# Kernel optimization log

Hardware: AMD Instinct MI355X
Metric: run time of the kernel (lower is better)

## Reference

```python
import jax, jax.numpy as jnp
import numpy as np

VOCAB, N_CLASS, H, E = 50000, 6, 512, 300
B, S = 256, 512


def setup_inputs() -> dict:
    key = jax.random.key(0)
    ks = jax.random.split(key, 10)
    return {
        "seq": jax.random.randint(ks[0], (B, S), 0, VOCAB),
        "classes": jnp.arange(N_CLASS),
        "embed_W": jax.random.normal(ks[1], (VOCAB, E), jnp.float32) * 0.1,
        "embed_class_W": jax.random.normal(ks[2], (N_CLASS, H), jnp.float32) * 0.1,
        "W_ih": jax.random.normal(ks[3], (3 * H, E), jnp.float32) * 0.05,
        "W_hh": jax.random.normal(ks[4], (3 * H, H), jnp.float32) * 0.05,
        "b_ih": jax.random.normal(ks[5], (3 * H,), jnp.float32) * 0.05,
        "b_hh": jax.random.normal(ks[6], (3 * H,), jnp.float32) * 0.05,
        "attend": jax.random.normal(ks[7], (H, H), jnp.float32) * 0.1,
        "W_cls": jax.random.normal(ks[8], (2, H), jnp.float32) * 0.05,
        "b_cls": jax.random.normal(ks[9], (2,), jnp.float32) * 0.05,
    }


def _gru_scan(xs, W_ih, W_hh, b_ih, b_hh):
    # xs: [S, B, E]; torch GRUCell semantics
    h0 = jnp.zeros((xs.shape[1], W_hh.shape[1]), xs.dtype)

    def step(h, x):
        gi = x @ W_ih.T + b_ih            # [B, 3H]
        gh = h @ W_hh.T + b_hh            # [B, 3H]
        i_r, i_z, i_n = jnp.split(gi, 3, axis=-1)
        h_r, h_z, h_n = jnp.split(gh, 3, axis=-1)
        r = jax.nn.sigmoid(i_r + h_r)
        z = jax.nn.sigmoid(i_z + h_z)
        n = jnp.tanh(i_n + r * h_n)
        h_new = (1.0 - z) * n + z * h
        return h_new, h_new

    _, hs = jax.lax.scan(step, h0, xs)
    return hs  # [S, B, H]


def reference(seq, classes, embed_W, embed_class_W, W_ih, W_hh, b_ih, b_hh,
              attend, W_cls, b_cls):
    pad_mask = (seq > 0).astype(embed_W.dtype)          # [B, S]
    seq_emb = jnp.tanh(embed_W[seq])                    # [B, S, E]
    hs = _gru_scan(seq_emb.transpose(1, 0, 2), W_ih, W_hh, b_ih, b_hh)
    seq_repr = hs.transpose(1, 0, 2)                    # [B, S, H]

    class_emb = embed_class_W[classes]                  # [C, H]
    attn = jnp.tanh(class_emb) @ attend                 # [C, H]
    # scores[c,b,s] = tanh(attn)[c] . seq_repr[b,s], masked
    scores = jnp.einsum('ch,bsh->cbs', jnp.tanh(attn), seq_repr)
    scores = scores * pad_mask[None, :, :]
    ctx = jnp.einsum('cbs,bsh->cbh', jnp.tanh(scores), seq_repr)  # [C, B, H]
    logits = jnp.tanh(ctx) @ W_cls.T + b_cls            # [C, B, 2]
    return jax.nn.log_softmax(logits, axis=-1)
```

## Files before the change

### kernel.cpp

```cpp
#include <hip/hip_runtime.h>
#include <cstdint>
#include <cstddef>

#define NB 256
#define NS 512
#define NE 300
#define NH 512

using f32x4 = __attribute__((ext_vector_type(4))) float;
using s16x8 = __attribute__((ext_vector_type(8))) short;

static __device__ __forceinline__ unsigned short f2bf(float f) {
  unsigned u = __float_as_uint(f);
  u += 0x7FFFu + ((u >> 16) & 1u);
  return (unsigned short)(u >> 16);
}
static __device__ __forceinline__ float bf2f(unsigned short h) {
  return __uint_as_float(((unsigned)h) << 16);
}
static __device__ __forceinline__ float fast_tanh(float x) {
  float xc = fminf(fmaxf(x, -9.f), 9.f);
  float e = __expf(2.f * xc);
  return (e - 1.f) / (e + 1.f);
}
static __device__ __forceinline__ float sigm(float x) {
  return 1.f / (1.f + __expf(-x));
}

__global__ void k_zero(unsigned short* __restrict__ h_ex, unsigned* __restrict__ flags) {
  int i = blockIdx.x * 256 + threadIdx.x;
  f32x4 z = {0.f, 0.f, 0.f, 0.f};
  *(f32x4*)(h_ex + (size_t)i * 16) = z;
  *(f32x4*)(h_ex + (size_t)i * 16 + 8) = z;
  if (i < 512) flags[i] = 0;
}

__global__ __launch_bounds__(256) void k_amat(const int* __restrict__ classes,
                                              const float* __restrict__ ecw,
                                              const float* __restrict__ attend,
                                              unsigned short* __restrict__ a_bf) {
  __shared__ float tc[6][512];
  const int tid = threadIdx.x, j = blockIdx.x;
  for (int i = tid; i < 6 * 512; i += 256) {
    int c = i >> 9, hp = i & 511;
    tc[c][hp] = fast_tanh(ecw[(size_t)classes[c] * 512 + hp]);
  }
  __syncthreads();
  #pragma unroll
  for (int i = 0; i < 4; ++i) {
    int task = tid + 256 * i;
    int c = task >> 6, hl = task & 63;
    int h = j * 64 + hl;
    float v = 0.f;
    if (c < 6) {
      float acc = 0.f;
      for (int hp = 0; hp < 512; ++hp) acc += tc[c][hp] * attend[(size_t)hp * 512 + h];
      v = fast_tanh(acc);
    }
    a_bf[c * 512 + h] = f2bf(v);
  }
}

__global__ __launch_bounds__(384) void k_gru(
    const int* __restrict__ seq, const float* __restrict__ embed_W,
    const float* __restrict__ W_ih, const float* __restrict__ W_hh,
    const float* __restrict__ b_ih, const float* __restrict__ b_hh,
    unsigned short* __restrict__ h_ex, unsigned* __restrict__ flags,
    unsigned short* __restrict__ seq_repr)
{
  __shared__ unsigned short x_lds[2][16][328];
  __shared__ unsigned short h_lds[16][520];
  __shared__ float rz_lds[2][16][32];

  const int tid = threadIdx.x;
  const int w = tid >> 6, l = tid & 63, lo = l & 15, hi = l >> 4;
  const int bid = blockIdx.x;
  const int g_b = (bid & 7) * 2 + (bid >> 7);
  const int g_c = (bid >> 3) & 15;

  const int gg = w >> 1;
  const int cb = (w & 1) * 16;
  const int jrow = gg * 512 + g_c * 32 + cb + lo;

  s16x8 whh[16];
  #pragma unroll
  for (int kt = 0; kt < 16; ++kt) {
    const float* p = W_hh + (size_t)jrow * 512 + kt * 32 + hi * 8;
    f32x4 a0 = *(const f32x4*)p;
    f32x4 a1 = *(const f32x4*)(p + 4);
    s16x8 v;
    v[0]=(short)f2bf(a0[0]); v[1]=(short)f2bf(a0[1]); v[2]=(short)f2bf(a0[2]); v[3]=(short)f2bf(a0[3]);
    v[4]=(short)f2bf(a1[0]); v[5]=(short)f2bf(a1[1]); v[6]=(short)f2bf(a1[2]); v[7]=(short)f2bf(a1[3]);
    whh[kt] = v;
  }
  s16x8 wih[10];
  #pragma unroll
  for (int kt = 0; kt < 10; ++kt) {
    s16x8 v;
    #pragma unroll
    for (int jj = 0; jj < 8; ++jj) {
      int k = kt * 32 + hi * 8 + jj;
      float f = (k < NE) ? W_ih[(size_t)jrow * NE + k] : 0.f;
      v[jj] = (short)f2bf(f);
    }
    wih[kt] = v;
  }
  const float bsum = b_ih[jrow] + b_hh[jrow];
  const float bni = b_ih[jrow], bnh = b_hh[jrow];

  float hcar[4] = {0.f, 0.f, 0.f, 0.f};
  const unsigned* flg = flags + g_b * 32;

  auto do_gather = [&](int ss) {
    const int buf = ss & 1;
    #pragma unroll
    for (int i = 0; i < 2; ++i) {
      int task = tid + 384 * i;
      if (task < 640) {
        int r = task & 15, grp = task >> 4;
        float vals[8];
        if (grp < 38) {
          int id = seq[(size_t)(g_b * 16 + r) * NS + ss];
          const float* ep = embed_W + (size_t)id * NE;
          if (grp < 37) {
            f32x4 u0 = *(const f32x4*)(ep + grp * 8);
            f32x4 u1 = *(const f32x4*)(ep + grp * 8 + 4);
            vals[0]=u0[0];vals[1]=u0[1];vals[2]=u0[2];vals[3]=u0[3];
            vals[4]=u1[0];vals[5]=u1[1];vals[6]=u1[2];vals[7]=u1[3];
          } else {
            #pragma unroll
            for (int jj = 0; jj < 8; ++jj) { int cc = 296 + jj; vals[jj] = (cc < NE) ? ep[cc] : 0.f; }
          }
        } else {
          #pragma unroll
          for (int jj = 0; jj < 8; ++jj) vals[jj] = 0.f;
        }
        s16x8 pv;
        #pragma unroll
        for (int jj = 0; jj < 8; ++jj) pv[jj] = (short)f2bf(fast_tanh(vals[jj]));
        *(s16x8*)&x_lds[buf][r][grp * 8] = pv;
      }
    }
  };

  do_gather(0);
  __syncthreads();

  #pragma unroll 1
  for (int s = 0; s < NS; ++s) {
    if (s + 1 < NS) do_gather(s + 1);

    f32x4 ax = {0.f,0.f,0.f,0.f};
    #pragma unroll
    for (int kt = 0; kt < 10; ++kt) {
      s16x8 af = *(const s16x8*)&x_lds[s & 1][lo][kt * 32 + hi * 8];
      ax = __builtin_amdgcn_mfma_f32_16x16x32_bf16(af, wih[kt], ax, 0, 0, 0);
    }

    if (s > 0 && tid < 64) {
      int guard = 0;
      for (;;) {
        unsigned f = __hip_atomic_load(flg + (l & 31),
                                       __ATOMIC_RELAXED, __HIP_MEMORY_SCOPE_AGENT);
        if (__all(f >= (unsigned)s)) break;
        __builtin_amdgcn_s_sleep(1);
        if (++guard > (1 << 24)) break;
      }
    }
    __syncthreads();

    const unsigned short* hsrc = h_ex + ((size_t)(s & 1) * 16 + g_b) * (16 * 512);
    #pragma unroll
    for (int i = 0; i < 6; ++i) {
      int task = tid + 384 * i;
      if (task < 2048) {
        int r = task >> 7, c4 = task & 127;
        unsigned long long v = __hip_atomic_load(
            (const unsigned long long*)(hsrc + r * 512 + c4 * 4),
            __ATOMIC_RELAXED, __HIP_MEMORY_SCOPE_AGENT);
        *(unsigned long long*)&h_lds[r][c4 * 4] = v;
      }
    }
    __syncthreads();

    f32x4 ah0 = {0.f,0.f,0.f,0.f}, ah1 = {0.f,0.f,0.f,0.f};
    #pragma unroll
    for (int kt = 0; kt < 16; kt += 2) {
      s16x8 af0 = *(const s16x8*)&h_lds[lo][kt * 32 + hi * 8];
      s16x8 af1 = *(const s16x8*)&h_lds[lo][(kt + 1) * 32 + hi * 8];
      ah0 = __builtin_amdgcn_mfma_f32_16x16x32_bf16(af0, whh[kt], ah0, 0, 0, 0);
      ah1 = __builtin_amdgcn_mfma_f32_16x16x32_bf16(af1, whh[kt + 1], ah1, 0, 0, 0);
    }
    f32x4 ah = ah0 + ah1;

    if (w < 4) {
      #pragma unroll
      for (int j = 0; j < 4; ++j) {
        int row = hi * 4 + j;
        rz_lds[gg][row][cb + lo] = ax[j] + ah[j] + bsum;
      }
    }
    __syncthreads();

    if (w >= 4) {
      unsigned short* hdst = h_ex + ((size_t)((s + 1) & 1) * 16 + g_b) * (16 * 512);
      const int cpr = cb + lo;
      const int col = g_c * 32 + cpr;
      unsigned words[4];
      #pragma unroll
      for (int j = 0; j < 4; ++j) {
        int row = hi * 4 + j;
        float rr = sigm(rz_lds[0][row][cpr]);
        float zz = sigm(rz_lds[1][row][cpr]);
        float nn = fast_tanh(ax[j] + bni + rr * (ah[j] + bnh));
        float hn = (1.f - zz) * nn + zz * hcar[j];
        hcar[j] = hn;
        unsigned myb = (unsigned)f2bf(hn);
        unsigned other = __shfl_xor(myb, 1);
        words[j] = myb | (other << 16);
      }
      if ((lo & 1) == 0) {
        #pragma unroll
        for (int j = 0; j < 4; ++j)
          __hip_atomic_store((unsigned*)(hdst + (hi * 4 + j) * 512 + col), words[j],
                             __ATOMIC_RELAXED, __HIP_MEMORY_SCOPE_AGENT);
      }
      asm volatile("s_waitcnt vmcnt(0)" ::: "memory");
      if (l == 0)
        __hip_atomic_store((unsigned*)(flags + g_b * 32 + g_c * 2 + (w & 1)),
                           (unsigned)(s + 1),
                           __ATOMIC_RELAXED, __HIP_MEMORY_SCOPE_AGENT);
      if ((lo & 1) == 0) {
        #pragma unroll
        for (int j = 0; j < 4; ++j)
          *(unsigned*)(seq_repr + ((size_t)(g_b * 16 + hi * 4 + j) * NS + s) * NH + col) = words[j];
      }
    }
  }
}

__global__ __launch_bounds__(256) void k_attn(const int* __restrict__ seq,
                                              const unsigned short* __restrict__ seq_repr,
                                              const unsigned short* __restrict__ a_bf,
                                              const float* __restrict__ W_cls,
                                              const float* __restrict__ b_cls,
                                              float* __restrict__ out)
{
  __shared__ unsigned short V[32][520];
  __shared__ float P[32][8];
  __shared__ float red[4][12];
  const int tid = threadIdx.x, b = blockIdx.x;
  const int w = tid >> 6, l = tid & 63, lo = l & 15, hi = l >> 4;

  s16x8 afr[16];
  #pragma unroll
  for (int kt = 0; kt < 16; ++kt)
    afr[kt] = *(const s16x8*)(a_bf + (size_t)lo * 512 + kt * 32 + hi * 8);

  float ctx0[6] = {0,0,0,0,0,0}, ctx1[6] = {0,0,0,0,0,0};
  const unsigned short* vbase = seq_repr + (size_t)b * NS * NH;

  for (int sc = 0; sc < 16; ++sc) {
    #pragma unroll 4
    for (int i = 0; i < 8; ++i) {
      int task = tid + 256 * i;
      int sl = task >> 6, grp = task & 63;
      s16x8 v = *(const s16x8*)(vbase + (size_t)(sc * 32 + sl) * NH + grp * 8);
      *(s16x8*)&V[sl][grp * 8] = v;
    }
    __syncthreads();
    if (w < 2) {
      f32x4 acc = {0.f,0.f,0.f,0.f};
      int sl0 = w * 16;
      #pragma unroll
      for (int kt = 0; kt < 16; ++kt) {
        s16x8 af = *(const s16x8*)&V[sl0 + lo][kt * 32 + hi * 8];
        acc = __builtin_amdgcn_mfma_f32_16x16x32_bf16(af, afr[kt], acc, 0, 0, 0);
      }
      if (lo < 8) {
        #pragma unroll
        for (int j = 0; j < 4; ++j) {
          int sl = sl0 + hi * 4 + j;
          float p = 0.f;
          if (lo < 6) {
            int s = sc * 32 + sl;
            p = (seq[(size_t)b * NS + s] > 0) ? fast_tanh(acc[j]) : 0.f;
          }
          P[sl][lo] = p;
        }
      }
    }
    __syncthreads();
    #pragma unroll 2
    for (int sl = 0; sl < 32; ++sl) {
      unsigned v2 = *(const unsigned*)&V[sl][tid * 2];
      float v0 = bf2f((unsigned short)(v2 & 0xFFFFu));
      float v1 = bf2f((unsigned short)(v2 >> 16));
      #pragma unroll
      for (int c = 0; c < 6; ++c) {
        float p = P[sl][c];
        ctx0[c] += p * v0; ctx1[c] += p * v1;
      }
    }
    __syncthreads();
  }

  float pl[12];
  #pragma unroll
  for (int c = 0; c < 6; ++c) {
    float t0 = fast_tanh(ctx0[c]), t1 = fast_tanh(ctx1[c]);
    pl[c * 2 + 0] = t0 * W_cls[tid * 2] + t1 * W_cls[tid * 2 + 1];
    pl[c * 2 + 1] = t0 * W_cls[512 + tid * 2] + t1 * W_cls[512 + tid * 2 + 1];
  }
  #pragma unroll
  for (int i = 0; i < 12; ++i) {
    float v = pl[i];
    for (int off = 32; off > 0; off >>= 1) v += __shfl_down(v, off);
    if (l == 0) red[w][i] = v;
  }
  __syncthreads();
  if (tid < 6) {
    int c = tid;
    float l0 = red[0][c*2] + red[1][c*2] + red[2][c*2] + red[3][c*2] + b_cls[0];
    float l1 = red[0][c*2+1] + red[1][c*2+1] + red[2][c*2+1] + red[3][c*2+1] + b_cls[1];
    float m = fmaxf(l0, l1);
    float lse = m + logf(__expf(l0 - m) + __expf(l1 - m));
    out[c * 512 + b * 2 + 0] = l0 - lse;
    out[c * 512 + b * 2 + 1] = l1 - lse;
  }
}

extern "C" void kernel_launch(void* const* d_in, const int* in_sizes, int n_in,
                              void* d_out, int out_size, void* d_ws, size_t ws_size,
                              hipStream_t stream) {
  const int*   seq      = (const int*)d_in[0];
  const int*   classes  = (const int*)d_in[1];
  const float* embed_W  = (const float*)d_in[2];
  const float* ecw      = (const float*)d_in[3];
  const float* W_ih     = (const float*)d_in[4];
  const float* W_hh     = (const float*)d_in[5];
  const float* b_ih     = (const float*)d_in[6];
  const float* b_hh     = (const float*)d_in[7];
  const float* attend   = (const float*)d_in[8];
  const float* W_cls    = (const float*)d_in[9];
  const float* b_cls    = (const float*)d_in[10];
  float* out = (float*)d_out;

  char* ws = (char*)d_ws;
  unsigned short* seq_repr = (unsigned short*)ws;
  unsigned short* h_ex     = (unsigned short*)(ws + 134217728);
  unsigned*       flags    = (unsigned*)(ws + 134217728 + 524288);
  unsigned short* a_bf     = (unsigned short*)(ws + 134217728 + 524288 + 2048);

  hipLaunchKernelGGL(k_zero, dim3(64), dim3(256), 0, stream, h_ex, flags);
  hipLaunchKernelGGL(k_amat, dim3(8), dim3(256), 0, stream, classes, ecw, attend, a_bf);
  hipLaunchKernelGGL(k_gru, dim3(256), dim3(384), 0, stream,
                     seq, embed_W, W_ih, W_hh, b_ih, b_hh, h_ex, flags, seq_repr);
  hipLaunchKernelGGL(k_attn, dim3(256), dim3(256), 0, stream,
                     seq, seq_repr, a_bf, W_cls, b_cls, out);
}
```

Before: 2.278 ms.

## Precompute tanh embeddings into bf16 staging buffer before the GRU scan

Adds a k_xemb kernel that gathers embedding rows, applies tanh, converts to bf16 and writes them into a workspace buffer laid out per batch group and timestep. The GRU kernel then streams these precomputed tiles into LDS with simple vector loads, replacing the in-loop random gather and transcendental math on the serial critical path. The cost is an extra pass writing and reading about 84 MB, and the fast path runs only when the workspace is large enough. The flag/zero kernel now uses atomic stores and the spin-wait timeout is shortened.

```diff
diff --git a/kernel.cpp b/kernel.cpp
--- a/kernel.cpp
+++ b/kernel.cpp
@@ -29,10 +29,47 @@
 
 __global__ void k_zero(unsigned short* __restrict__ h_ex, unsigned* __restrict__ flags) {
   int i = blockIdx.x * 256 + threadIdx.x;
-  f32x4 z = {0.f, 0.f, 0.f, 0.f};
-  *(f32x4*)(h_ex + (size_t)i * 16) = z;
-  *(f32x4*)(h_ex + (size_t)i * 16 + 8) = z;
-  if (i < 512) flags[i] = 0;
+  unsigned long long* p = (unsigned long long*)(h_ex + (size_t)i * 16);
+  #pragma unroll
+  for (int j = 0; j < 4; ++j)
+    __hip_atomic_store(p + j, 0ull, __ATOMIC_RELAXED, __HIP_MEMORY_SCOPE_AGENT);
+  if (i < 4096)
+    __hip_atomic_store(flags + i, 0u, __ATOMIC_RELAXED, __HIP_MEMORY_SCOPE_AGENT);
+}
+
+__global__ __launch_bounds__(256) void k_xemb(const int* __restrict__ seq,
+                                              const float* __restrict__ embed_W,
+                                              unsigned short* __restrict__ x_pre) {
+  const long long total = (long long)NB * NS * 40;
+  for (long long t = (long long)blockIdx.x * 256 + threadIdx.x; t < total;
+       t += (long long)gridDim.x * 256) {
+    int c = (int)(t % 40);
+    long long p = t / 40;
+    int s = (int)(p % NS);
+    int b = (int)(p / NS);
+    int g_b = b >> 4, r = b & 15;
+    float vals[8];
+    if (c < 38) {
+      int id = seq[(size_t)b * NS + s];
+      const float* ep = embed_W + (size_t)id * NE;
+      if (c < 37) {
+        f32x4 u0 = *(const f32x4*)(ep + c * 8);
+        f32x4 u1 = *(const f32x4*)(ep + c * 8 + 4);
+        vals[0]=u0[0];vals[1]=u0[1];vals[2]=u0[2];vals[3]=u0[3];
+        vals[4]=u1[0];vals[5]=u1[1];vals[6]=u1[2];vals[7]=u1[3];
+      } else {
+        #pragma unroll
+        for (int jj = 0; jj < 8; ++jj) { int cc = 296 + jj; vals[jj] = (cc < NE) ? ep[cc] : 0.f; }
+      }
+    } else {
+      #pragma unroll
+      for (int jj = 0; jj < 8; ++jj) vals[jj] = 0.f;
+    }
+    s16x8 pv;
+    #pragma unroll
+    for (int jj = 0; jj < 8; ++jj) pv[jj] = (short)f2bf(fast_tanh(vals[jj]));
+    *(s16x8*)(x_pre + (((size_t)g_b * NS + s) * 16 + r) * 320 + c * 8) = pv;
+  }
 }
 
 __global__ __launch_bounds__(256) void k_amat(const int* __restrict__ classes,
@@ -66,7 +103,8 @@
     const float* __restrict__ W_ih, const float* __restrict__ W_hh,
     const float* __restrict__ b_ih, const float* __restrict__ b_hh,
     unsigned short* __restrict__ h_ex, unsigned* __restrict__ flags,
-    unsigned short* __restrict__ seq_repr)
+    unsigned short* __restrict__ seq_repr,
+    const unsigned short* __restrict__ x_pre, int xpre)
 {
   __shared__ unsigned short x_lds[2][16][328];
   __shared__ unsigned short h_lds[16][520];
@@ -110,6 +148,20 @@
 
   float hcar[4] = {0.f, 0.f, 0.f, 0.f};
   const unsigned* flg = flags + g_b * 32;
+
+  const int xt = tid - 64;
+  const int xr0 = (xt >= 0) ? (xt / 40) : 0,          xc0 = (xt >= 0) ? (xt % 40) : 0;
+  const int xr1 = (xt >= 0) ? ((xt + 320) / 40) : 0,  xc1 = (xt >= 0) ? ((xt + 320) % 40) : 0;
+
+  auto do_xload = [&](int ss) {
+    if (w >= 1) {
+      const unsigned short* src = x_pre + ((size_t)g_b * NS + ss) * (16 * 320);
+      s16x8 v0 = *(const s16x8*)(src + xr0 * 320 + xc0 * 8);
+      s16x8 v1 = *(const s16x8*)(src + xr1 * 320 + xc1 * 8);
+      *(s16x8*)&x_lds[ss & 1][xr0][xc0 * 8] = v0;
+      *(s16x8*)&x_lds[ss & 1][xr1][xc1 * 8] = v1;
+    }
+  };
 
   auto do_gather = [&](int ss) {
     const int buf = ss & 1;
@@ -143,12 +195,14 @@
     }
   };
 
-  do_gather(0);
+  if (xpre) do_xload(0); else do_gather(0);
   __syncthreads();
 
   #pragma unroll 1
   for (int s = 0; s < NS; ++s) {
-    if (s + 1 < NS) do_gather(s + 1);
+    if (s + 1 < NS) {
+      if (xpre) do_xload(s + 1); else do_gather(s + 1);
+    }
 
     f32x4 ax = {0.f,0.f,0.f,0.f};
     #pragma unroll
@@ -158,13 +212,13 @@
     }
 
     if (s > 0 && tid < 64) {
+      const unsigned* fp = flg + (l & 31);
       int guard = 0;
       for (;;) {
-        unsigned f = __hip_atomic_load(flg + (l & 31),
-                                       __ATOMIC_RELAXED, __HIP_MEMORY_SCOPE_AGENT);
+        unsigned f = __hip_atomic_load(fp, __ATOMIC_RELAXED, __HIP_MEMORY_SCOPE_AGENT);
         if (__all(f >= (unsigned)s)) break;
         __builtin_amdgcn_s_sleep(1);
-        if (++guard > (1 << 24)) break;
+        if (++guard > (1 << 22)) break;
       }
     }
     __syncthreads();
@@ -347,15 +401,25 @@
   float* out = (float*)d_out;
 
   char* ws = (char*)d_ws;
+  const size_t OFF_HEX  = 134217728;
+  const size_t OFF_FLG  = OFF_HEX + 524288;
+  const size_t OFF_ABF  = OFF_FLG + 16384;
+  const size_t OFF_XPRE = OFF_ABF + 16384;
+  const size_t XPRE_BYTES = (size_t)16 * NS * 16 * 320 * 2;
   unsigned short* seq_repr = (unsigned short*)ws;
-  unsigned short* h_ex     = (unsigned short*)(ws + 134217728);
-  unsigned*       flags    = (unsigned*)(ws + 134217728 + 524288);
-  unsigned short* a_bf     = (unsigned short*)(ws + 134217728 + 524288 + 2048);
+  unsigned short* h_ex     = (unsigned short*)(ws + OFF_HEX);
+  unsigned*       flags    = (unsigned*)(ws + OFF_FLG);
+  unsigned short* a_bf     = (unsigned short*)(ws + OFF_ABF);
+  unsigned short* x_pre    = (unsigned short*)(ws + OFF_XPRE);
+  const int xpre = (ws_size >= OFF_XPRE + XPRE_BYTES) ? 1 : 0;
 
   hipLaunchKernelGGL(k_zero, dim3(64), dim3(256), 0, stream, h_ex, flags);
   hipLaunchKernelGGL(k_amat, dim3(8), dim3(256), 0, stream, classes, ecw, attend, a_bf);
+  if (xpre)
+    hipLaunchKernelGGL(k_xemb, dim3(2048), dim3(256), 0, stream, seq, embed_W, x_pre);
   hipLaunchKernelGGL(k_gru, dim3(256), dim3(384), 0, stream,
-                     seq, embed_W, W_ih, W_hh, b_ih, b_hh, h_ex, flags, seq_repr);
+                     seq, embed_W, W_ih, W_hh, b_ih, b_hh, h_ex, flags, seq_repr,
+                     x_pre, xpre);
   hipLaunchKernelGGL(k_attn, dim3(256), dim3(256), 0, stream,
                      seq, seq_repr, a_bf, W_cls, b_cls, out);
 }
```

Result: faster. 2.225 ms (-2.3%).
